# Optimization experiments

Hardware: AMD Instinct MI355X
Metric: run time of the kernel (lower is better)

## Reference

```python
import jax, jax.numpy as jnp
import numpy as np

N_EMBD = 2048
N_HEAD = 16
HEAD_DIM = N_EMBD // N_HEAD
ROPE_THETA = 10000.0


def _rope_cache(seq_len, head_dim, theta):
    inv_freq = 1.0 / theta ** (jnp.arange(0, head_dim, 2, dtype=jnp.float32) / head_dim)
    t = jnp.arange(seq_len, dtype=jnp.float32)
    freqs = jnp.outer(t, inv_freq)  # [S, head_dim//2]
    return jnp.cos(freqs), jnp.sin(freqs)


def _apply_rope(x, cos, sin):
    # x: [B, H, S, D]; cos/sin: [S, D//2] -> broadcast over B, H
    cos = cos[None, None, :, :]
    sin = sin[None, None, :, :]
    x1 = x[..., ::2]
    x2 = x[..., 1::2]
    rot = jnp.stack((x1 * cos - x2 * sin, x1 * sin + x2 * cos), axis=-1)
    return rot.reshape(x.shape)


def setup_inputs() -> dict:
    key = jax.random.key(0)
    ks = jax.random.split(key, 5)
    scale = 1.0 / np.sqrt(N_EMBD)
    x = jax.random.normal(ks[0], (2, 2048, N_EMBD), dtype=jnp.float32)
    wq = jax.random.normal(ks[1], (N_EMBD, N_EMBD), dtype=jnp.float32) * scale
    wk = jax.random.normal(ks[2], (N_EMBD, N_EMBD), dtype=jnp.float32) * scale
    wv = jax.random.normal(ks[3], (N_EMBD, N_EMBD), dtype=jnp.float32) * scale
    wo = jax.random.normal(ks[4], (N_EMBD, N_EMBD), dtype=jnp.float32) * scale
    return {"x": x, "wq": wq, "wk": wk, "wv": wv, "wo": wo}


def reference(x, wq, wk, wv, wo):
    bsz, seq_len, _ = x.shape
    q = (x @ wq).reshape(bsz, seq_len, N_HEAD, HEAD_DIM).transpose(0, 2, 1, 3)
    k = (x @ wk).reshape(bsz, seq_len, N_HEAD, HEAD_DIM).transpose(0, 2, 1, 3)
    v = (x @ wv).reshape(bsz, seq_len, N_HEAD, HEAD_DIM).transpose(0, 2, 1, 3)

    cos, sin = _rope_cache(seq_len, HEAD_DIM, ROPE_THETA)
    q = _apply_rope(q, cos, sin)
    k = _apply_rope(k, cos, sin)

    scale = 1.0 / np.sqrt(HEAD_DIM)
    att = jnp.einsum('bhqd,bhkd->bhqk', q, k) * scale  # [B,H,S,S]
    causal = jnp.tril(jnp.ones((seq_len, seq_len), dtype=bool))
    att = jnp.where(causal[None, None, :, :], att, -jnp.inf)
    att = jax.nn.softmax(att, axis=-1)
    y = jnp.einsum('bhqk,bhkd->bhqd', att, v)  # [B,H,S,D]
    y = y.transpose(0, 2, 1, 3).reshape(bsz, seq_len, N_EMBD)
    return y @ wo
```

## Files before the change

### kernel.cpp

```cpp
#include <hip/hip_runtime.h>
#include <math.h>

constexpr int BSZ = 2;
constexpr int SEQ = 2048;
constexpr int NE  = 2048;
constexpr int NH  = 16;
constexpr int HD  = 128;
constexpr int MROWS = BSZ * SEQ;

typedef __bf16 bf16x8 __attribute__((ext_vector_type(8)));
typedef float  f32x4  __attribute__((ext_vector_type(4)));

__device__ __forceinline__ unsigned short f2bf(float f) {
    union { float f; unsigned u; } v; v.f = f;
    unsigned r = v.u + 0x7fffu + ((v.u >> 16) & 1u);
    return (unsigned short)(r >> 16);
}
__device__ __forceinline__ float bf2f(unsigned short s) {
    union { unsigned u; float f; } v; v.u = ((unsigned)s) << 16; return v.f;
}

__device__ __forceinline__ void load_lds16(const void* g, void* l) {
    __builtin_amdgcn_global_load_lds(
        (const __attribute__((address_space(1))) unsigned int*)g,
        (__attribute__((address_space(3))) unsigned int*)l, 16, 0, 0);
}

template <int CTRL>
__device__ __forceinline__ float dpp_mv(float x) {
    int v = __builtin_amdgcn_update_dpp(
        0, __builtin_bit_cast(int, x), CTRL, 0xF, 0xF, true);
    return __builtin_bit_cast(float, v);
}
__device__ __forceinline__ float row16_max(float x) {
    x = fmaxf(x, dpp_mv<0xB1>(x));
    x = fmaxf(x, dpp_mv<0x4E>(x));
    x = fmaxf(x, dpp_mv<0x124>(x));
    x = fmaxf(x, dpp_mv<0x128>(x));
    return x;
}
__device__ __forceinline__ float row16_sum(float x) {
    x += dpp_mv<0xB1>(x);
    x += dpp_mv<0x4E>(x);
    x += dpp_mv<0x124>(x);
    x += dpp_mv<0x128>(x);
    return x;
}

__global__ __launch_bounds__(256) void transpose_cast(const float* __restrict__ xf,
                                                      const float* __restrict__ w0,
                                                      const float* __restrict__ w1,
                                                      const float* __restrict__ w2,
                                                      const float* __restrict__ w3,
                                                      ushort* __restrict__ xb,
                                                      ushort* __restrict__ o0,
                                                      ushort* __restrict__ o1,
                                                      ushort* __restrict__ o2,
                                                      ushort* __restrict__ o3)
{
    if (blockIdx.z == 4) {
        const int tid = threadIdx.y * 32 + threadIdx.x;
        const size_t i = (((size_t)blockIdx.y * 64 + blockIdx.x) * 256 + tid) * 8;
        float4 v0 = *(const float4*)(xf + i);
        float4 v1 = *(const float4*)(xf + i + 4);
        ushort4 a, b;
        a.x = f2bf(v0.x); a.y = f2bf(v0.y); a.z = f2bf(v0.z); a.w = f2bf(v0.w);
        b.x = f2bf(v1.x); b.y = f2bf(v1.y); b.z = f2bf(v1.z); b.w = f2bf(v1.w);
        *(ushort4*)(xb + i)     = a;
        *(ushort4*)(xb + i + 4) = b;
        return;
    }

    const float* S; ushort* D;
    switch (blockIdx.z) {
        case 0: S = w0; D = o0; break;
        case 1: S = w1; D = o1; break;
        case 2: S = w2; D = o2; break;
        default: S = w3; D = o3; break;
    }
    __shared__ float t[32][33];
    const int tx = threadIdx.x, ty = threadIdx.y;
    const int x0 = blockIdx.x * 32, y0 = blockIdx.y * 32;
#pragma unroll
    for (int i = 0; i < 4; ++i)
        t[ty + i * 8][tx] = S[(size_t)(y0 + ty + i * 8) * NE + x0 + tx];
    __syncthreads();
#pragma unroll
    for (int i = 0; i < 4; ++i)
        D[(size_t)(x0 + ty + i * 8) * NE + y0 + tx] = f2bf(t[tx][ty + i * 8]);
}

__global__ __launch_bounds__(256) void gemm_qkv(const ushort* __restrict__ A,
                                                const ushort* __restrict__ W,
                                                ushort* __restrict__ Qb,
                                                ushort* __restrict__ Kb,
                                                ushort* __restrict__ Vt)
{
    __shared__ ushort Al[128 * 64];
    __shared__ ushort Bl[128 * 64];

    const int tid  = threadIdx.x;
    const int w    = tid >> 6;
    const int lane = tid & 63;
    const int quad = lane >> 4;
    const int r    = lane & 15;
    const int wm   = w & 1;
    const int wn   = w >> 1;
    const int m0 = blockIdx.y * 128;
    const int n0 = blockIdx.x * 128;
    const int K  = NE;

    const int srow = tid >> 3;
    const int scol = ((tid & 7) ^ ((tid >> 3) & 7)) * 8;

    f32x4 acc[4][4] = {};

    for (int k0 = 0; k0 < K; k0 += 64) {
#pragma unroll
        for (int j = 0; j < 4; ++j) {
            load_lds16(A + (size_t)(m0 + j * 32 + srow) * K + k0 + scol,
                       &Al[j * 2048 + w * 512]);
            load_lds16(W + (size_t)(n0 + j * 32 + srow) * K + k0 + scol,
                       &Bl[j * 2048 + w * 512]);
        }
        __syncthreads();

#pragma unroll
        for (int kh = 0; kh < 2; ++kh) {
            const int sw = (((kh << 2) + quad) ^ (r & 7)) * 8;
            bf16x8 af[4], bfr[4];
#pragma unroll
            for (int it = 0; it < 4; ++it)
                af[it] = *(const bf16x8*)&Al[(wm * 64 + it * 16 + r) * 64 + sw];
#pragma unroll
            for (int jt = 0; jt < 4; ++jt)
                bfr[jt] = *(const bf16x8*)&Bl[(wn * 64 + jt * 16 + r) * 64 + sw];
#pragma unroll
            for (int it = 0; it < 4; ++it)
#pragma unroll
                for (int jt = 0; jt < 4; ++jt)
                    acc[it][jt] = __builtin_amdgcn_mfma_f32_16x16x32_bf16(
                        af[it], bfr[jt], acc[it][jt], 0, 0, 0);
        }
        __syncthreads();
    }

    const int mat  = n0 >> 11;
    const int ncol = n0 & 2047;
    if (mat < 2) {
        ushort* C = mat ? Kb : Qb;
        float invf[4];
#pragma unroll
        for (int jt = 0; jt < 4; ++jt) {
            const int d = (wn * 64 + jt * 16 + r) & 127;
            invf[jt] = exp2f((float)(d >> 1) * -0.20762050593046014f);
        }
        const float sgn = (r & 1) ? 1.0f : -1.0f;
#pragma unroll
        for (int it = 0; it < 4; ++it) {
            const int row = m0 + wm * 64 + it * 16 + quad * 4;
#pragma unroll
            for (int jt = 0; jt < 4; ++jt) {
                const int col = ncol + wn * 64 + jt * 16 + r;
#pragma unroll
                for (int reg = 0; reg < 4; ++reg) {
                    const float self = acc[it][jt][reg];
                    const float part = dpp_mv<0xB1>(self);
                    const int s = (row + reg) & 2047;
                    const float f = (float)s * invf[jt];
                    const float sn = __sinf(f);
                    const float cs = __cosf(f);
                    const float y = self * cs + sgn * part * sn;
                    C[(size_t)(row + reg) * NE + col] = f2bf(y);
                }
            }
        }
    } else {
#pragma unroll
        for (int it = 0; it < 4; ++it) {
            const int row = m0 + wm * 64 + it * 16 + quad * 4;
            const int bb = row >> 11;
            const int s  = row & 2047;
#pragma unroll
            for (int jt = 0; jt < 4; ++jt) {
                const int col = ncol + wn * 64 + jt * 16 + r;
                const int hh = col >> 7;
                const int d  = col & 127;
                ushort4 pk;
                pk.x = f2bf(acc[it][jt][0]); pk.y = f2bf(acc[it][jt][1]);
                pk.z = f2bf(acc[it][jt][2]); pk.w = f2bf(acc[it][jt][3]);
                *(ushort4*)&Vt[((size_t)((bb * NH + hh) * HD + d)) * SEQ + s] = pk;
            }
        }
    }
}

__global__ __launch_bounds__(256) void gemm_out(const ushort* __restrict__ A,
                                                const ushort* __restrict__ Bt,
                                                float* __restrict__ C)
{
    __shared__ ushort Al[128 * 64];
    __shared__ ushort Bl[128 * 64];

    const int tid  = threadIdx.x;
    const int w    = tid >> 6;
    const int lane = tid & 63;
    const int quad = lane >> 4;
    const int r    = lane & 15;
    const int wm   = w & 1;
    const int wn   = w >> 1;
    const int m0 = blockIdx.y * 128;
    const int n0 = blockIdx.x * 128;
    const int K  = NE;

    const int srow = tid >> 3;
    const int scol = ((tid & 7) ^ ((tid >> 3) & 7)) * 8;

    f32x4 acc[4][4] = {};

    for (int k0 = 0; k0 < K; k0 += 64) {
#pragma unroll
        for (int j = 0; j < 4; ++j) {
            load_lds16(A  + (size_t)(m0 + j * 32 + srow) * K + k0 + scol,
                       &Al[j * 2048 + w * 512]);
            load_lds16(Bt + (size_t)(n0 + j * 32 + srow) * K + k0 + scol,
                       &Bl[j * 2048 + w * 512]);
        }
        __syncthreads();

#pragma unroll
        for (int kh = 0; kh < 2; ++kh) {
            const int sw = (((kh << 2) + quad) ^ (r & 7)) * 8;
            bf16x8 af[4], bfr[4];
#pragma unroll
            for (int it = 0; it < 4; ++it)
                af[it] = *(const bf16x8*)&Al[(wm * 64 + it * 16 + r) * 64 + sw];
#pragma unroll
            for (int jt = 0; jt < 4; ++jt)
                bfr[jt] = *(const bf16x8*)&Bl[(wn * 64 + jt * 16 + r) * 64 + sw];
#pragma unroll
            for (int it = 0; it < 4; ++it)
#pragma unroll
                for (int jt = 0; jt < 4; ++jt)
                    acc[it][jt] = __builtin_amdgcn_mfma_f32_16x16x32_bf16(
                        af[it], bfr[jt], acc[it][jt], 0, 0, 0);
        }
        __syncthreads();
    }

#pragma unroll
    for (int it = 0; it < 4; ++it) {
        const int row = m0 + wm * 64 + it * 16 + quad * 4;
#pragma unroll
        for (int jt = 0; jt < 4; ++jt) {
            const int col = n0 + wn * 64 + jt * 16 + r;
#pragma unroll
            for (int reg = 0; reg < 4; ++reg)
                C[(size_t)(row + reg) * NE + col] = acc[it][jt][reg];
        }
    }
}

__global__ __launch_bounds__(256, 2) void flash_attn(const ushort* __restrict__ Qg,
                                                     const ushort* __restrict__ Kg,
                                                     const ushort* __restrict__ Vtg,
                                                     ushort* __restrict__ Yg)
{
    const int qt = (int)gridDim.x - 1 - (int)blockIdx.x;
    const int bh = blockIdx.y;
    const int b = bh >> 4, h = bh & 15;
    const int tid  = threadIdx.x;
    const int w    = tid >> 6;
    const int lane = tid & 63;
    const int quad = lane >> 4;
    const int r    = lane & 15;

    __shared__ ushort Ks[64][136];
    __shared__ ushort Vts[128][72];
    __shared__ ushort Ps[64][72];

    const int q0 = qt * 64;
    const size_t qkbase = (size_t)b * SEQ * NE + (size_t)h * HD;
    const size_t vbase  = (size_t)(bh * HD) * SEQ;
    const float scale = 0.088388347648318447f;

    bf16x8 aq[4];
    {
        const ushort* qrow = Qg + qkbase + (size_t)(q0 + w * 16 + r) * NE;
#pragma unroll
        for (int kc = 0; kc < 4; ++kc)
            aq[kc] = *(const bf16x8*)(qrow + kc * 32 + quad * 8);
    }

    float m_i[4], l_i[4];
    f32x4 acc_o[8];
#pragma unroll
    for (int reg = 0; reg < 4; ++reg) { m_i[reg] = -INFINITY; l_i[reg] = 0.f; }
#pragma unroll
    for (int dt = 0; dt < 8; ++dt) acc_o[dt] = f32x4{0.f, 0.f, 0.f, 0.f};

    for (int t = 0; t <= qt; ++t) {
        const int j0 = t * 64;

        {
            const int row0 = tid >> 4;
            const int ch   = (tid & 15) * 8;
#pragma unroll
            for (int i = 0; i < 4; ++i) {
                const int row = i * 16 + row0;
                *(uint4*)&Ks[row][ch] =
                    *(const uint4*)(Kg + qkbase + (size_t)(j0 + row) * NE + ch);
            }
            const int d0  = tid >> 3;
            const int ch2 = (tid & 7) * 8;
#pragma unroll
            for (int i = 0; i < 4; ++i) {
                const int d = i * 32 + d0;
                *(uint4*)&Vts[d][ch2] =
                    *(const uint4*)(Vtg + vbase + (size_t)d * SEQ + j0 + ch2);
            }
        }
        __syncthreads();

        __builtin_amdgcn_s_setprio(1);
        f32x4 sa[4];
#pragma unroll
        for (int jt = 0; jt < 4; ++jt) {
            f32x4 acc = {0.f, 0.f, 0.f, 0.f};
#pragma unroll
            for (int kc = 0; kc < 4; ++kc) {
                bf16x8 bk = *(const bf16x8*)&Ks[jt * 16 + r][kc * 32 + quad * 8];
                acc = __builtin_amdgcn_mfma_f32_16x16x32_bf16(aq[kc], bk, acc, 0, 0, 0);
            }
            sa[jt] = acc;
        }
        __builtin_amdgcn_s_setprio(0);

        if (t == qt) {
#pragma unroll
            for (int jt = 0; jt < 4; ++jt)
#pragma unroll
                for (int reg = 0; reg < 4; ++reg)
                    sa[jt][reg] = (jt * 16 + r > w * 16 + quad * 4 + reg)
                                  ? -INFINITY : sa[jt][reg] * scale;
        } else {
#pragma unroll
            for (int jt = 0; jt < 4; ++jt)
#pragma unroll
                for (int reg = 0; reg < 4; ++reg)
                    sa[jt][reg] *= scale;
        }

        float rmax[4], alpha[4], rsum[4];
#pragma unroll
        for (int reg = 0; reg < 4; ++reg) {
            rmax[reg] = fmaxf(fmaxf(sa[0][reg], sa[1][reg]),
                              fmaxf(sa[2][reg], sa[3][reg]));
            rmax[reg] = row16_max(rmax[reg]);
        }

#pragma unroll
        for (int reg = 0; reg < 4; ++reg) {
            const float mnew = fmaxf(m_i[reg], rmax[reg]);
            alpha[reg] = __expf(m_i[reg] - mnew);
            m_i[reg] = mnew;
            rsum[reg] = 0.f;
        }
#pragma unroll
        for (int jt = 0; jt < 4; ++jt)
#pragma unroll
            for (int reg = 0; reg < 4; ++reg) {
                const float p = __expf(sa[jt][reg] - m_i[reg]);
                sa[jt][reg] = p;
                rsum[reg] += p;
            }
#pragma unroll
        for (int reg = 0; reg < 4; ++reg) {
            rsum[reg] = row16_sum(rsum[reg]);
            l_i[reg] = l_i[reg] * alpha[reg] + rsum[reg];
        }

#pragma unroll
        for (int jt = 0; jt < 4; ++jt)
#pragma unroll
            for (int reg = 0; reg < 4; ++reg)
                Ps[w * 16 + quad * 4 + reg][jt * 16 + r] = f2bf(sa[jt][reg]);

#pragma unroll
        for (int dt = 0; dt < 8; ++dt)
#pragma unroll
            for (int reg = 0; reg < 4; ++reg)
                acc_o[dt][reg] *= alpha[reg];

        bf16x8 ap[2];
#pragma unroll
        for (int kc = 0; kc < 2; ++kc)
            ap[kc] = *(const bf16x8*)&Ps[w * 16 + r][kc * 32 + quad * 8];
        __builtin_amdgcn_s_setprio(1);
#pragma unroll
        for (int dt = 0; dt < 8; ++dt)
#pragma unroll
            for (int kc = 0; kc < 2; ++kc) {
                bf16x8 bv = *(const bf16x8*)&Vts[dt * 16 + r][kc * 32 + quad * 8];
                acc_o[dt] = __builtin_amdgcn_mfma_f32_16x16x32_bf16(ap[kc], bv, acc_o[dt], 0, 0, 0);
            }
        __builtin_amdgcn_s_setprio(0);
        __syncthreads();
    }

#pragma unroll
    for (int reg = 0; reg < 4; ++reg) {
        const float inv = 1.0f / l_i[reg];
        const size_t rowbase = qkbase + (size_t)(q0 + w * 16 + quad * 4 + reg) * NE;
#pragma unroll
        for (int dt = 0; dt < 8; ++dt)
            Yg[rowbase + dt * 16 + r] = f2bf(acc_o[dt][reg] * inv);
    }
}

extern "C" void kernel_launch(void* const* d_in, const int* in_sizes, int n_in,
                              void* d_out, int out_size, void* d_ws, size_t ws_size,
                              hipStream_t stream)
{
    const float* x  = (const float*)d_in[0];
    const float* wq = (const float*)d_in[1];
    const float* wk = (const float*)d_in[2];
    const float* wv = (const float*)d_in[3];
    const float* wo = (const float*)d_in[4];
    float* out = (float*)d_out;

    ushort* ws = (ushort*)d_ws;
    const size_t MAT  = (size_t)MROWS * NE;
    const size_t WMAT = (size_t)NE * NE;
    ushort* xb  = ws;
    ushort* wqT = xb + MAT;
    ushort* wkT = wqT + WMAT;
    ushort* wvT = wkT + WMAT;
    ushort* woT = wvT + WMAT;
    ushort* Qb  = woT + WMAT;
    ushort* Kb  = Qb + MAT;
    ushort* Vt  = Kb + MAT;
    ushort* Yb  = Qb;

    transpose_cast<<<dim3(64, 64, 5), dim3(32, 8), 0, stream>>>(
        x, wq, wk, wv, wo, xb, wqT, wkT, wvT, woT);

    gemm_qkv<<<dim3(48, 32), 256, 0, stream>>>(xb, wqT, Qb, Kb, Vt);

    flash_attn<<<dim3(SEQ / 64, BSZ * NH), 256, 0, stream>>>(Qb, Kb, Vt, Yb);

    gemm_out<<<dim3(16, 32), 256, 0, stream>>>(Yb, woT, out);
}
```

Measured before the change: 437.0 us.

## Process two 64-row query sub-tiles per attention block to share K/V tiles

```diff
diff --git a/kernel.cpp b/kernel.cpp
--- a/kernel.cpp
+++ b/kernel.cpp
@@ -266,7 +266,7 @@
                                                      const ushort* __restrict__ Vtg,
                                                      ushort* __restrict__ Yg)
 {
-    const int qt = (int)gridDim.x - 1 - (int)blockIdx.x;
+    const int qb = (int)gridDim.x - 1 - (int)blockIdx.x;
     const int bh = blockIdx.y;
     const int b = bh >> 4, h = bh & 15;
     const int tid  = threadIdx.x;
@@ -279,27 +279,33 @@
     __shared__ ushort Vts[128][72];
     __shared__ ushort Ps[64][72];
 
-    const int q0 = qt * 64;
+    const int q0 = qb * 128;
     const size_t qkbase = (size_t)b * SEQ * NE + (size_t)h * HD;
     const size_t vbase  = (size_t)(bh * HD) * SEQ;
     const float scale = 0.088388347648318447f;
 
-    bf16x8 aq[4];
-    {
-        const ushort* qrow = Qg + qkbase + (size_t)(q0 + w * 16 + r) * NE;
+    bf16x8 aq[2][4];
+#pragma unroll
+    for (int s = 0; s < 2; ++s) {
+        const ushort* qrow = Qg + qkbase + (size_t)(q0 + s * 64 + w * 16 + r) * NE;
 #pragma unroll
         for (int kc = 0; kc < 4; ++kc)
-            aq[kc] = *(const bf16x8*)(qrow + kc * 32 + quad * 8);
-    }
-
-    float m_i[4], l_i[4];
-    f32x4 acc_o[8];
-#pragma unroll
-    for (int reg = 0; reg < 4; ++reg) { m_i[reg] = -INFINITY; l_i[reg] = 0.f; }
-#pragma unroll
-    for (int dt = 0; dt < 8; ++dt) acc_o[dt] = f32x4{0.f, 0.f, 0.f, 0.f};
-
-    for (int t = 0; t <= qt; ++t) {
+            aq[s][kc] = *(const bf16x8*)(qrow + kc * 32 + quad * 8);
+    }
+
+    float m_i[2][4], l_i[2][4];
+    f32x4 acc_o[2][8];
+#pragma unroll
+    for (int s = 0; s < 2; ++s)
+#pragma unroll
+        for (int reg = 0; reg < 4; ++reg) { m_i[s][reg] = -INFINITY; l_i[s][reg] = 0.f; }
+#pragma unroll
+    for (int s = 0; s < 2; ++s)
+#pragma unroll
+        for (int dt = 0; dt < 8; ++dt) acc_o[s][dt] = f32x4{0.f, 0.f, 0.f, 0.f};
+
+    const int ntiles = 2 * qb + 2;
+    for (int t = 0; t < ntiles; ++t) {
         const int j0 = t * 64;
 
         {
@@ -322,100 +328,110 @@
         }
         __syncthreads();
 
-        __builtin_amdgcn_s_setprio(1);
-        f32x4 sa[4];
-#pragma unroll
-        for (int jt = 0; jt < 4; ++jt) {
-            f32x4 acc = {0.f, 0.f, 0.f, 0.f};
-#pragma unroll
-            for (int kc = 0; kc < 4; ++kc) {
-                bf16x8 bk = *(const bf16x8*)&Ks[jt * 16 + r][kc * 32 + quad * 8];
-                acc = __builtin_amdgcn_mfma_f32_16x16x32_bf16(aq[kc], bk, acc, 0, 0, 0);
-            }
-            sa[jt] = acc;
-        }
-        __builtin_amdgcn_s_setprio(0);
-
-        if (t == qt) {
+#pragma unroll
+        for (int s = 0; s < 2; ++s) {
+            const int diag = 2 * qb + s;
+            if (t > diag) continue;
+
+            __builtin_amdgcn_s_setprio(1);
+            f32x4 sa[4];
+#pragma unroll
+            for (int jt = 0; jt < 4; ++jt) {
+                f32x4 acc = {0.f, 0.f, 0.f, 0.f};
+#pragma unroll
+                for (int kc = 0; kc < 4; ++kc) {
+                    bf16x8 bk = *(const bf16x8*)&Ks[jt * 16 + r][kc * 32 + quad * 8];
+                    acc = __builtin_amdgcn_mfma_f32_16x16x32_bf16(aq[s][kc], bk, acc, 0, 0, 0);
+                }
+                sa[jt] = acc;
+            }
+            __builtin_amdgcn_s_setprio(0);
+
+            if (t == diag) {
+#pragma unroll
+                for (int jt = 0; jt < 4; ++jt)
+#pragma unroll
+                    for (int reg = 0; reg < 4; ++reg)
+                        sa[jt][reg] = (jt * 16 + r > w * 16 + quad * 4 + reg)
+                                      ? -INFINITY : sa[jt][reg] * scale;
+            } else {
+#pragma unroll
+                for (int jt = 0; jt < 4; ++jt)
+#pragma unroll
+                    for (int reg = 0; reg < 4; ++reg)
+                        sa[jt][reg] *= scale;
+            }
+
+            float rmax[4], alpha[4], rsum[4];
+#pragma unroll
+            for (int reg = 0; reg < 4; ++reg) {
+                rmax[reg] = fmaxf(fmaxf(sa[0][reg], sa[1][reg]),
+                                  fmaxf(sa[2][reg], sa[3][reg]));
+                rmax[reg] = row16_max(rmax[reg]);
+            }
+
+#pragma unroll
+            for (int reg = 0; reg < 4; ++reg) {
+                const float mnew = fmaxf(m_i[s][reg], rmax[reg]);
+                alpha[reg] = __expf(m_i[s][reg] - mnew);
+                m_i[s][reg] = mnew;
+                rsum[reg] = 0.f;
+            }
 #pragma unroll
             for (int jt = 0; jt < 4; ++jt)
 #pragma unroll
+                for (int reg = 0; reg < 4; ++reg) {
+                    const float p = __expf(sa[jt][reg] - m_i[s][reg]);
+                    sa[jt][reg] = p;
+                    rsum[reg] += p;
+                }
+#pragma unroll
+            for (int reg = 0; reg < 4; ++reg) {
+                rsum[reg] = row16_sum(rsum[reg]);
+                l_i[s][reg] = l_i[s][reg] * alpha[reg] + rsum[reg];
+            }
+
+#pragma unroll
+            for (int jt = 0; jt < 4; ++jt)
+#pragma unroll
                 for (int reg = 0; reg < 4; ++reg)
-                    sa[jt][reg] = (jt * 16 + r > w * 16 + quad * 4 + reg)
-                                  ? -INFINITY : sa[jt][reg] * scale;
-        } else {
-#pragma unroll
-            for (int jt = 0; jt < 4; ++jt)
+                    Ps[w * 16 + quad * 4 + reg][jt * 16 + r] = f2bf(sa[jt][reg]);
+
+#pragma unroll
+            for (int dt = 0; dt < 8; ++dt)
 #pragma unroll
                 for (int reg = 0; reg < 4; ++reg)
-                    sa[jt][reg] *= scale;
-        }
-
-        float rmax[4], alpha[4], rsum[4];
+                    acc_o[s][dt][reg] *= alpha[reg];
+
+            bf16x8 ap[2];
+#pragma unroll
+            for (int kc = 0; kc < 2; ++kc)
+                ap[kc] = *(const bf16x8*)&Ps[w * 16 + r][kc * 32 + quad * 8];
+            __builtin_amdgcn_s_setprio(1);
+#pragma unroll
+            for (int dt = 0; dt < 8; ++dt)
+#pragma unroll
+                for (int kc = 0; kc < 2; ++kc) {
+                    bf16x8 bv = *(const bf16x8*)&Vts[dt * 16 + r][kc * 32 + quad * 8];
+                    acc_o[s][dt] = __builtin_amdgcn_mfma_f32_16x16x32_bf16(
+                        ap[kc], bv, acc_o[s][dt], 0, 0, 0);
+                }
+            __builtin_amdgcn_s_setprio(0);
+        }
+        __syncthreads();
+    }
+
+#pragma unroll
+    for (int s = 0; s < 2; ++s)
 #pragma unroll
         for (int reg = 0; reg < 4; ++reg) {
-            rmax[reg] = fmaxf(fmaxf(sa[0][reg], sa[1][reg]),
-                              fmaxf(sa[2][reg], sa[3][reg]));
-            rmax[reg] = row16_max(rmax[reg]);
-        }
-
-#pragma unroll
-        for (int reg = 0; reg < 4; ++reg) {
-            const float mnew = fmaxf(m_i[reg], rmax[reg]);
-            alpha[reg] = __expf(m_i[reg] - mnew);
-            m_i[reg] = mnew;
-            rsum[reg] = 0.f;
-        }
-#pragma unroll
-        for (int jt = 0; jt < 4; ++jt)
-#pragma unroll
-            for (int reg = 0; reg < 4; ++reg) {
-                const float p = __expf(sa[jt][reg] - m_i[reg]);
-                sa[jt][reg] = p;
-                rsum[reg] += p;
-            }
-#pragma unroll
-        for (int reg = 0; reg < 4; ++reg) {
-            rsum[reg] = row16_sum(rsum[reg]);
-            l_i[reg] = l_i[reg] * alpha[reg] + rsum[reg];
-        }
-
-#pragma unroll
-        for (int jt = 0; jt < 4; ++jt)
-#pragma unroll
-            for (int reg = 0; reg < 4; ++reg)
-                Ps[w * 16 + quad * 4 + reg][jt * 16 + r] = f2bf(sa[jt][reg]);
-
-#pragma unroll
-        for (int dt = 0; dt < 8; ++dt)
-#pragma unroll
-            for (int reg = 0; reg < 4; ++reg)
-                acc_o[dt][reg] *= alpha[reg];
-
-        bf16x8 ap[2];
-#pragma unroll
-        for (int kc = 0; kc < 2; ++kc)
-            ap[kc] = *(const bf16x8*)&Ps[w * 16 + r][kc * 32 + quad * 8];
-        __builtin_amdgcn_s_setprio(1);
-#pragma unroll
-        for (int dt = 0; dt < 8; ++dt)
-#pragma unroll
-            for (int kc = 0; kc < 2; ++kc) {
-                bf16x8 bv = *(const bf16x8*)&Vts[dt * 16 + r][kc * 32 + quad * 8];
-                acc_o[dt] = __builtin_amdgcn_mfma_f32_16x16x32_bf16(ap[kc], bv, acc_o[dt], 0, 0, 0);
-            }
-        __builtin_amdgcn_s_setprio(0);
-        __syncthreads();
-    }
-
-#pragma unroll
-    for (int reg = 0; reg < 4; ++reg) {
-        const float inv = 1.0f / l_i[reg];
-        const size_t rowbase = qkbase + (size_t)(q0 + w * 16 + quad * 4 + reg) * NE;
-#pragma unroll
-        for (int dt = 0; dt < 8; ++dt)
-            Yg[rowbase + dt * 16 + r] = f2bf(acc_o[dt][reg] * inv);
-    }
+            const float inv = 1.0f / l_i[s][reg];
+            const size_t rowbase =
+                qkbase + (size_t)(q0 + s * 64 + w * 16 + quad * 4 + reg) * NE;
+#pragma unroll
+            for (int dt = 0; dt < 8; ++dt)
+                Yg[rowbase + dt * 16 + r] = f2bf(acc_o[s][dt][reg] * inv);
+        }
 }
 
 extern "C" void kernel_launch(void* const* d_in, const int* in_sizes, int n_in,
@@ -447,7 +463,7 @@
 
     gemm_qkv<<<dim3(48, 32), 256, 0, stream>>>(xb, wqT, Qb, Kb, Vt);
 
-    flash_attn<<<dim3(SEQ / 64, BSZ * NH), 256, 0, stream>>>(Qb, Kb, Vt, Yb);
+    flash_attn<<<dim3(SEQ / 128, BSZ * NH), 256, 0, stream>>>(Qb, Kb, Vt, Yb);
 
     gemm_out<<<dim3(16, 32), 256, 0, stream>>>(Yb, woT, out);
 }
```

Measured after the change: 473.1 us. 1.08x slower.
